# Kernel tuning notes

Hardware: AMD Instinct MI355X
Metric: run time of the kernel (lower is better)

The kernel has to match this reference:

```python
import jax, jax.numpy as jnp
import numpy as np

IN_SIZE = 512
UNITS = 512
GRID_SIZE = 5
ORDER = 3
LO, HI = -1.0, 1.0
BATCH = 1024


def _make_grid():
    # grid: (in_size, grid_size + 2*order + 1), extended beyond grid_range by order knot spacings
    bound = HI - LO
    g = jnp.linspace(LO - ORDER * bound / GRID_SIZE,
                     HI + ORDER * bound / GRID_SIZE,
                     GRID_SIZE + 2 * ORDER + 1, dtype=jnp.float32)
    return jnp.tile(g[None, :], (IN_SIZE, 1))


def _spline_bases(x, grid):
    # Cox-de Boor recursion. x: (B, in), grid: (in, G)
    xe = x[..., None]  # (B, in, 1)
    bases = ((xe >= grid[:, :-1]) & (xe < grid[:, 1:])).astype(x.dtype)  # order-0 indicators
    for k in range(1, ORDER + 1):
        left = (xe - grid[:, :-(k + 1)]) / (grid[:, k:-1] - grid[:, :-(k + 1)]) * bases[..., :-1]
        right = (grid[:, k + 1:] - xe) / (grid[:, k + 1:] - grid[:, 1:-k]) * bases[..., 1:]
        bases = left + right
    return bases  # (B, in, grid_size + order)


def setup_inputs() -> dict:
    key = jax.random.key(0)
    k1, k2, k3 = jax.random.split(key, 3)
    x = jax.random.normal(k1, (BATCH, IN_SIZE), jnp.float32)
    spline_kernel = 0.1 * jax.random.normal(k2, (IN_SIZE, GRID_SIZE + ORDER, UNITS), jnp.float32)
    limit = float(np.sqrt(6.0 / (IN_SIZE + UNITS)))  # GlorotUniform
    scale_factor = jax.random.uniform(k3, (IN_SIZE, UNITS), jnp.float32, -limit, limit)
    bias = jnp.zeros((UNITS,), jnp.float32)
    return {"x": x, "spline_kernel": spline_kernel, "scale_factor": scale_factor, "bias": bias}


def reference(x, spline_kernel, scale_factor, bias):
    grid = _make_grid()
    bases = _spline_bases(x, grid)                              # (B, in, basis)
    spline_out = jnp.einsum('bik,iko->bio', bases, spline_kernel)  # (B, in, units)
    spline_out = spline_out + jax.nn.silu(x)[..., None]            # add basis activation per feature
    spline_out = spline_out * scale_factor[None]                   # per (in, units) scaling
    out = jnp.sum(spline_out, axis=-2) + bias                      # reduce over in_size
    return out
```

## Files before the change

kernel.cpp:

```cpp
#include <hip/hip_runtime.h>
#include <cstdint>
#include <cmath>

typedef unsigned short u16;
typedef __bf16 bf16x8 __attribute__((ext_vector_type(8)));
typedef float f32x4 __attribute__((ext_vector_type(4)));

#define B_SZ   1024
#define IN_SZ  512
#define U_SZ   512
#define KTOT   4608
#define SPLITS 8
#define KLEN   576
#define BK     32
#define KITERS 18

__device__ __forceinline__ u16 f2bf(float f) {
  __bf16 h = (__bf16)f;
  return __builtin_bit_cast(u16, h);
}

__device__ __forceinline__ void async16(const void* g, void* l) {
  __builtin_amdgcn_global_load_lds(
      (__attribute__((address_space(1))) void*)(g),
      (__attribute__((address_space(3))) void*)(l), 16u, 0, 0u);
}

__global__ void __launch_bounds__(256) prep_all(const float* __restrict__ SK,
                                                const float* __restrict__ SF,
                                                const float* __restrict__ X,
                                                u16* __restrict__ WT,
                                                u16* __restrict__ A) {
  const int bx = blockIdx.x;
  const int tid = threadIdx.x;

  if (bx < 512) {
    __shared__ u16 tile[72 * 66];
    const int o0 = (bx & 7) * 64;
    const int i0 = (bx >> 3) * 8;
    const int oo = tid & 63, grp = tid >> 6;
    for (int tr = grp; tr < 72; tr += 4) {
      int i = i0 + tr / 9;
      int k = tr % 9;
      float sf = SF[(size_t)i * U_SZ + o0 + oo];
      float v  = (k < 8) ? SK[((size_t)i * 8 + k) * U_SZ + o0 + oo] * sf : sf;
      tile[tr * 66 + oo] = f2bf(v);
    }
    __syncthreads();
    const int t0 = i0 * 9;
    for (int idx = tid; idx < 72 * 64; idx += 256) {
      int ol = idx / 72;
      int c  = idx - ol * 72;
      WT[(size_t)(o0 + ol) * KTOT + t0 + c] = tile[c * 66 + ol];
    }
  } else {
    __shared__ u16 st[2304];
    const int gid0 = (bx - 512) * 256;
    const float x = X[gid0 + tid];

    const float T0 = -2.2f, H = 0.4f;
    float b0[11], b1[10], b2[9], b3[8];
#pragma unroll
    for (int j = 0; j < 11; ++j) {
      float tj  = T0 + H * j;
      float tj1 = T0 + H * (j + 1);
      b0[j] = (x >= tj && x < tj1) ? 1.0f : 0.0f;
    }
#pragma unroll
    for (int j = 0; j < 10; ++j) {
      float tj  = T0 + H * j;
      float tj2 = T0 + H * (j + 2);
      b1[j] = (x - tj) * 2.5f * b0[j] + (tj2 - x) * 2.5f * b0[j + 1];
    }
#pragma unroll
    for (int j = 0; j < 9; ++j) {
      float tj  = T0 + H * j;
      float tj3 = T0 + H * (j + 3);
      b2[j] = (x - tj) * 1.25f * b1[j] + (tj3 - x) * 1.25f * b1[j + 1];
    }
#pragma unroll
    for (int j = 0; j < 8; ++j) {
      float tj  = T0 + H * j;
      float tj4 = T0 + H * (j + 4);
      b3[j] = (x - tj) * (1.0f / 1.2f) * b2[j] + (tj4 - x) * (1.0f / 1.2f) * b2[j + 1];
    }
    float sil = x / (1.0f + expf(-x));

#pragma unroll
    for (int k = 0; k < 8; ++k) st[tid * 9 + k] = f2bf(b3[k]);
    st[tid * 9 + 8] = f2bf(sil);
    __syncthreads();
    u16* dst = A + (size_t)gid0 * 9;
#pragma unroll
    for (int j = 0; j < 9; ++j) dst[j * 256 + tid] = st[j * 256 + tid];
  }
}

__global__ void __launch_bounds__(256) gemm_kan(const u16* __restrict__ A,
                                                const u16* __restrict__ WT,
                                                float* __restrict__ P) {
  __shared__ __align__(16) u16 sA[2][128 * BK];
  __shared__ __align__(16) u16 sB[2][128 * BK];

  const int t    = threadIdx.x;
  const int lane = t & 63;
  const int w    = t >> 6;
  const int wr   = w >> 1;
  const int wn   = w & 1;
  const int m0   = blockIdx.x * 128;
  const int n0   = blockIdx.y * 128;
  const int kbase = blockIdx.z * KLEN;

  const int srow = t >> 2, sc = t & 3;
  const int sg0 = (sc ^ (srow & 3)) * 8;
  const int srow1 = (t + 256) >> 2, sc1 = t & 3;
  const int sg1 = (sc1 ^ (srow1 & 3)) * 8;
  const u16* gA0 = A  + (size_t)(m0 + srow)  * KTOT + sg0;
  const u16* gA1 = A  + (size_t)(m0 + srow1) * KTOT + sg1;
  const u16* gB0 = WT + (size_t)(n0 + srow)  * KTOT + sg0;
  const u16* gB1 = WT + (size_t)(n0 + srow1) * KTOT + sg1;

  f32x4 acc[4][4];
#pragma unroll
  for (int i = 0; i < 4; ++i)
#pragma unroll
    for (int j = 0; j < 4; ++j) acc[i][j] = (f32x4)0.0f;

  auto stage = [&](int buf, int k0) {
    char* lA = (char*)(&sA[buf][0]) + t * 16;
    char* lB = (char*)(&sB[buf][0]) + t * 16;
    async16(gA0 + k0, lA);
    async16(gA1 + k0, lA + 4096);
    async16(gB0 + k0, lB);
    async16(gB1 + k0, lB + 4096);
  };

  stage(0, kbase);

  const int m = lane & 15, q = lane >> 4;
  const int qs = (q ^ (m & 3)) * 16;
  const char* fA = (const char*)(&sA[0][0]) + (wr * 64 + m) * (BK * 2) + qs;
  const char* fB = (const char*)(&sB[0][0]) + (wn * 64 + m) * (BK * 2) + qs;
  const int bufstep = 128 * BK * 2;

#pragma unroll
  for (int it = 0; it < KITERS; ++it) {
    const int cur = it & 1;
    __syncthreads();
    if (it + 1 < KITERS) stage(cur ^ 1, kbase + (it + 1) * BK);

    bf16x8 af[4], bfv[4];
#pragma unroll
    for (int tt = 0; tt < 4; ++tt)
      af[tt] = *(const bf16x8*)(fA + cur * bufstep + tt * 16 * (BK * 2));
#pragma unroll
    for (int tt = 0; tt < 4; ++tt)
      bfv[tt] = *(const bf16x8*)(fB + cur * bufstep + tt * 16 * (BK * 2));
#pragma unroll
    for (int mt = 0; mt < 4; ++mt)
#pragma unroll
      for (int nt = 0; nt < 4; ++nt)
        acc[mt][nt] = __builtin_amdgcn_mfma_f32_16x16x32_bf16(
            af[mt], bfv[nt], acc[mt][nt], 0, 0, 0);
  }

  float* Pp = P + (size_t)blockIdx.z * (B_SZ * U_SZ);
#pragma unroll
  for (int mt = 0; mt < 4; ++mt)
#pragma unroll
    for (int rr = 0; rr < 4; ++rr) {
      int row = m0 + wr * 64 + mt * 16 + q * 4 + rr;
      size_t rb = (size_t)row * U_SZ + n0 + wn * 64 + m;
#pragma unroll
      for (int nt = 0; nt < 4; ++nt) Pp[rb + nt * 16] = acc[mt][nt][rr];
    }
}

__global__ void reduce_kernel(const float* __restrict__ P,
                              const float* __restrict__ bias,
                              float* __restrict__ out) {
  const int idx = blockIdx.x * 256 + threadIdx.x;
  const f32x4* P4 = (const f32x4*)P;
  f32x4 acc = P4[idx];
#pragma unroll
  for (int s = 1; s < SPLITS; ++s) acc += P4[(size_t)s * (B_SZ * U_SZ / 4) + idx];
  acc += ((const f32x4*)bias)[idx & 127];
  ((f32x4*)out)[idx] = acc;
}

extern "C" void kernel_launch(void* const* d_in, const int* in_sizes, int n_in,
                              void* d_out, int out_size, void* d_ws, size_t ws_size,
                              hipStream_t stream) {
  const float* X    = (const float*)d_in[0];
  const float* SK   = (const float*)d_in[1];
  const float* SF   = (const float*)d_in[2];
  const float* bias = (const float*)d_in[3];

  char* ws = (char*)d_ws;
  u16*   WT = (u16*)ws;
  u16*   A  = (u16*)(ws + 4718592);
  float* P  = (float*)(ws + 4718592 + 9437184);

  hipLaunchKernelGGL(prep_all,      dim3(2560),    dim3(256), 0, stream, SK, SF, X, WT, A);
  hipLaunchKernelGGL(gemm_kan,      dim3(8, 4, 8), dim3(256), 0, stream, A, WT, P);
  hipLaunchKernelGGL(reduce_kernel, dim3(512),     dim3(256), 0, stream, P, bias, (float*)d_out);
}
```

Baseline: 92.41 us.

## Fuse split-K reduction into GEMM via last-block atomic counter

Removes the separate reduce kernel. Each GEMM block bumps an atomic counter for its output tile after writing its partial sums, and the block that finishes last sums all split-K partials, adds the bias and writes the output. The counters are zeroed in the prep kernel. This saves one kernel launch and lets the reduction overlap with other GEMM blocks, at the cost of threadfence and atomics and a serialized tail done by the last blocks only.

New measurement: 107.0 us. +15.7%, slower.

```diff
diff --git a/kernel.cpp b/kernel.cpp
--- a/kernel.cpp
+++ b/kernel.cpp
@@ -30,11 +30,13 @@
                                                 const float* __restrict__ SF,
                                                 const float* __restrict__ X,
                                                 u16* __restrict__ WT,
-                                                u16* __restrict__ A) {
+                                                u16* __restrict__ A,
+                                                int* __restrict__ cnt) {
   const int bx = blockIdx.x;
   const int tid = threadIdx.x;
 
   if (bx < 512) {
+    if (bx == 0 && tid < 32) cnt[tid] = 0;
     __shared__ u16 tile[72 * 66];
     const int o0 = (bx & 7) * 64;
     const int i0 = (bx >> 3) * 8;
@@ -98,9 +100,13 @@
 
 __global__ void __launch_bounds__(256) gemm_kan(const u16* __restrict__ A,
                                                 const u16* __restrict__ WT,
-                                                float* __restrict__ P) {
+                                                const float* __restrict__ bias,
+                                                float* __restrict__ P,
+                                                int* __restrict__ cnt,
+                                                float* __restrict__ out) {
   __shared__ __align__(16) u16 sA[2][128 * BK];
   __shared__ __align__(16) u16 sB[2][128 * BK];
+  __shared__ int s_last;
 
   const int t    = threadIdx.x;
   const int lane = t & 63;
@@ -174,18 +180,32 @@
 #pragma unroll
       for (int nt = 0; nt < 4; ++nt) Pp[rb + nt * 16] = acc[mt][nt][rr];
     }
-}
-
-__global__ void reduce_kernel(const float* __restrict__ P,
-                              const float* __restrict__ bias,
-                              float* __restrict__ out) {
-  const int idx = blockIdx.x * 256 + threadIdx.x;
-  const f32x4* P4 = (const f32x4*)P;
-  f32x4 acc = P4[idx];
-#pragma unroll
-  for (int s = 1; s < SPLITS; ++s) acc += P4[(size_t)s * (B_SZ * U_SZ / 4) + idx];
-  acc += ((const f32x4*)bias)[idx & 127];
-  ((f32x4*)out)[idx] = acc;
+
+  __syncthreads();
+  if (t == 0) {
+    __threadfence();
+    s_last = atomicAdd(&cnt[blockIdx.x * 4 + blockIdx.y], 1);
+  }
+  __syncthreads();
+  if (s_last == SPLITS - 1) {
+    __threadfence();
+    const f32x4* P4 = (const f32x4*)P;
+    const f32x4* b4 = (const f32x4*)bias;
+    f32x4* o4 = (f32x4*)out;
+    const int cb = n0 >> 2;
+#pragma unroll
+    for (int j = 0; j < 16; ++j) {
+      int idx = j * 256 + t;
+      int r   = idx >> 5;
+      int c4  = idx & 31;
+      size_t e = (size_t)(m0 + r) * (U_SZ / 4) + cb + c4;
+      f32x4 v = b4[cb + c4];
+#pragma unroll
+      for (int z = 0; z < SPLITS; ++z)
+        v += P4[(size_t)z * (B_SZ * U_SZ / 4) + e];
+      o4[e] = v;
+    }
+  }
 }
 
 extern "C" void kernel_launch(void* const* d_in, const int* in_sizes, int n_in,
@@ -197,11 +217,11 @@
   const float* bias = (const float*)d_in[3];
 
   char* ws = (char*)d_ws;
-  u16*   WT = (u16*)ws;
-  u16*   A  = (u16*)(ws + 4718592);
-  float* P  = (float*)(ws + 4718592 + 9437184);
-
-  hipLaunchKernelGGL(prep_all,      dim3(2560),    dim3(256), 0, stream, SK, SF, X, WT, A);
-  hipLaunchKernelGGL(gemm_kan,      dim3(8, 4, 8), dim3(256), 0, stream, A, WT, P);
-  hipLaunchKernelGGL(reduce_kernel, dim3(512),     dim3(256), 0, stream, P, bias, (float*)d_out);
-}
+  u16*   WT  = (u16*)ws;
+  u16*   A   = (u16*)(ws + 4718592);
+  float* P   = (float*)(ws + 4718592 + 9437184);
+  int*   cnt = (int*)(ws + 4718592 + 9437184 + 16777216);
+
+  hipLaunchKernelGGL(prep_all, dim3(2560),    dim3(256), 0, stream, SK, SF, X, WT, A, cnt);
+  hipLaunchKernelGGL(gemm_kan, dim3(8, 4, 8), dim3(256), 0, stream, A, WT, bias, P, cnt, (float*)d_out);
+}
```
